# Performance work log

Hardware: AMD Instinct MI355X
Metric: run time of the kernel (lower is better)

## Reference

```python
import jax, jax.numpy as jnp
import numpy as np

B, T, C, H = 4, 4096, 1024, 64  # batch, seq_len, embedding_dimension, head_size


def setup_inputs() -> dict:
    key = jax.random.key(0)
    kx, kq, kk, kv = jax.random.split(key, 4)
    x = jax.random.normal(kx, (B, T, C), dtype=jnp.float32)
    # nn.Linear(C, H, bias=False) -> weight applied as x @ W with W:[C,H]
    s = 1.0 / np.sqrt(C)
    Wq = jax.random.normal(kq, (C, H), dtype=jnp.float32) * s
    Wk = jax.random.normal(kk, (C, H), dtype=jnp.float32) * s
    Wv = jax.random.normal(kv, (C, H), dtype=jnp.float32) * s
    return {"x": x, "Wq": Wq, "Wk": Wk, "Wv": Wv}


def reference(x, Wq, Wk, Wv):
    Bx, Tx, Cx = x.shape
    q = x @ Wq  # [B,T,H]
    k = x @ Wk  # [B,T,H]
    v = x @ Wv  # [B,T,H]
    # NOTE: original scales by C**-0.5 (embedding dim), not head_size**-0.5
    wei = jnp.einsum('bqh,bkh->bqk', q, k) * (Cx ** -0.5)  # [B,T,T]
    causal = jnp.tril(jnp.ones((Tx, Tx), dtype=bool))
    wei = jnp.where(causal, wei, -jnp.inf)
    wei = jax.nn.softmax(wei, axis=-1)
    out = jnp.einsum('bqk,bkh->bqh', wei, v)  # [B,T,H]
    return out
```

## Files before the change

kernel.cpp:

```cpp
#include <hip/hip_runtime.h>
#include <math.h>

#define BATCH 4
#define SEQ   4096
#define EMB   1024
#define HDIM  64
#define NSPLIT 4

typedef __attribute__((ext_vector_type(8))) short bf16x8;
typedef __attribute__((ext_vector_type(4))) float f32x4;
typedef __attribute__((ext_vector_type(4))) unsigned int u32x4;

#define MFMA16(a, b, c) __builtin_amdgcn_mfma_f32_16x16x32_bf16(a, b, c, 0, 0, 0)

__device__ __forceinline__ unsigned short f2bf(float f) {
  unsigned int u = __float_as_uint(f);
  u = (u + 0x7FFFu + ((u >> 16) & 1u)) >> 16;
  return (unsigned short)u;
}

__device__ __forceinline__ float fexp2(float x) {
  float r;
  asm("v_exp_f32 %0, %1" : "=v"(r) : "v"(x));
  return r;
}

__global__ __launch_bounds__(256) void wt_kernel(
    const float* __restrict__ Wq, const float* __restrict__ Wk,
    const float* __restrict__ Wv, unsigned short* __restrict__ wt) {
  __shared__ float tile[64][65];
  const int bid = blockIdx.x;
  const int m = bid >> 4, kt = bid & 15;
  const float* W = (m == 0) ? Wq : (m == 1) ? Wk : Wv;
  const int tid = threadIdx.x;
  {
    const int r = tid >> 2, c4 = tid & 3;
    const float* src = W + (size_t)(kt * 64 + r) * 64 + c4 * 16;
#pragma unroll
    for (int j = 0; j < 4; ++j) {
      float4 a = *(const float4*)(src + j * 4);
      tile[r][c4 * 16 + j * 4 + 0] = a.x;
      tile[r][c4 * 16 + j * 4 + 1] = a.y;
      tile[r][c4 * 16 + j * 4 + 2] = a.z;
      tile[r][c4 * 16 + j * 4 + 3] = a.w;
    }
  }
  __syncthreads();
  {
    const int col = tid >> 2, kq = tid & 3;
    unsigned short o[16];
#pragma unroll
    for (int j = 0; j < 16; ++j) o[j] = f2bf(tile[kq * 16 + j][col]);
    unsigned short* dst = wt + (size_t)(m * 64 + col) * 1024 + kt * 64 + kq * 16;
    *(bf16x8*)(dst)     = *(bf16x8*)&o[0];
    *(bf16x8*)(dst + 8) = *(bf16x8*)&o[8];
  }
}

__global__ __launch_bounds__(512) void qkv_mfma_kernel(
    const float* __restrict__ x, const unsigned short* __restrict__ wt,
    unsigned short* __restrict__ qb, unsigned short* __restrict__ kb,
    unsigned short* __restrict__ vt) {
  __shared__ __align__(16) unsigned short xs[64 * 64];
  __shared__ __align__(16) unsigned short ws[192 * 64];
  const int tid  = threadIdx.x;
  const int lane = tid & 63, wid = tid >> 6;
  const int g = lane >> 4, p = lane & 15;
  const int mt = wid >> 2, wq = wid & 3;
  const size_t row0 = (size_t)blockIdx.x * 64;

  const int sr = tid >> 3, sc = tid & 7;
  const float* xp = x + (row0 + sr) * EMB + sc * 8;

  f32x4 acc[2][3];
#pragma unroll
  for (int rt = 0; rt < 2; ++rt)
#pragma unroll
    for (int ct = 0; ct < 3; ++ct) acc[rt][ct] = (f32x4){0.f, 0.f, 0.f, 0.f};

  float4 rx[2];
  bf16x8 rw[3];
#pragma unroll
  for (int j = 0; j < 2; ++j) rx[j] = *(const float4*)(xp + j * 4);
#pragma unroll
  for (int it = 0; it < 3; ++it) {
    int i = tid + it * 512, col = i >> 3, cc = i & 7;
    rw[it] = *(const bf16x8*)(wt + (size_t)col * 1024 + cc * 8);
  }

  for (int kc = 0; kc < 16; ++kc) {
    __syncthreads();
#pragma unroll
    for (int j = 0; j < 2; ++j) {
      ushort4 h;
      h.x = f2bf(rx[j].x); h.y = f2bf(rx[j].y);
      h.z = f2bf(rx[j].z); h.w = f2bf(rx[j].w);
      *(ushort4*)((char*)xs + ((sr * 128 + sc * 16 + j * 8) ^ ((sr & 7) << 4))) = h;
    }
#pragma unroll
    for (int it = 0; it < 3; ++it) {
      int i = tid + it * 512, col = i >> 3, cc = i & 7;
      *(bf16x8*)((char*)ws + ((col * 128 + cc * 16) ^ ((col & 7) << 4))) = rw[it];
    }
    if (kc < 15) {
      const float* xpn = xp + (kc + 1) * 64;
#pragma unroll
      for (int j = 0; j < 2; ++j) rx[j] = *(const float4*)(xpn + j * 4);
#pragma unroll
      for (int it = 0; it < 3; ++it) {
        int i = tid + it * 512, col = i >> 3, cc = i & 7;
        rw[it] = *(const bf16x8*)(wt + (size_t)col * 1024 + (kc + 1) * 64 + cc * 8);
      }
    }
    __syncthreads();
#pragma unroll
    for (int ks = 0; ks < 2; ++ks) {
      bf16x8 af[2];
#pragma unroll
      for (int rt = 0; rt < 2; ++rt) {
        int row = mt * 32 + rt * 16 + p;
        af[rt] = *(const bf16x8*)((char*)xs +
                 ((row * 128 + ks * 64 + g * 16) ^ ((row & 7) << 4)));
      }
#pragma unroll
      for (int ct = 0; ct < 3; ++ct) {
        int col = wq * 48 + ct * 16 + p;
        bf16x8 bfr = *(const bf16x8*)((char*)ws +
                     ((col * 128 + ks * 64 + g * 16) ^ ((col & 7) << 4)));
#pragma unroll
        for (int rt = 0; rt < 2; ++rt)
          acc[rt][ct] = MFMA16(af[rt], bfr, acc[rt][ct]);
      }
    }
  }

  const int b     = (int)(row0 >> 12);
  const int tbase = (int)(row0 & 4095);
  unsigned short* vtb = vt + (((size_t)b * 64 + (tbase >> 6)) * 64) * 64;
#pragma unroll
  for (int rt = 0; rt < 2; ++rt)
#pragma unroll
    for (int ct = 0; ct < 3; ++ct) {
      const int c0  = wq * 48 + ct * 16;
      const int mtx = c0 >> 6;
      const int col = (c0 & 63) + p;
#pragma unroll
      for (int r = 0; r < 4; ++r) {
        const int row = mt * 32 + rt * 16 + 4 * g + r;
        const float vf = acc[rt][ct][r];
        if (mtx == 0)      qb[(row0 + row) * HDIM + col] = f2bf(vf * 0.0450843714f);
        else if (mtx == 1) kb[(row0 + row) * HDIM + col] = f2bf(vf);
        else               vtb[(size_t)col * 64 + row]   = f2bf(vf);
      }
    }
}

__device__ __forceinline__ void tile_body_lds(
    const unsigned short* __restrict__ sKb, const unsigned short* __restrict__ sVb,
    int qrel, bool diag,
    const bf16x8& qf0, const bf16x8& qf1,
    int p, int g, int cA0, int cA1, int srcA, int srcB, bool hi,
    float& m, float& l, f32x4 (&o)[4]) {
  f32x4 sc4[4];
#pragma unroll
  for (int t = 0; t < 4; ++t) {
    const int row = 16 * t + p;
    bf16x8 a0 = *(const bf16x8*)((const char*)sKb + row * 128 + cA0);
    bf16x8 a1 = *(const bf16x8*)((const char*)sKb + row * 128 + cA1);
    f32x4 a = (f32x4){0.f, 0.f, 0.f, 0.f};
    a = MFMA16(a0, qf0, a);
    a = MFMA16(a1, qf1, a);
    sc4[t] = a;
  }
  if (diag) {
#pragma unroll
    for (int t = 0; t < 4; ++t)
#pragma unroll
      for (int r = 0; r < 4; ++r)
        if (16 * t + 4 * g + r > qrel) sc4[t][r] = -1e30f;
  }
  float tm = -3e38f;
#pragma unroll
  for (int t = 0; t < 4; ++t)
#pragma unroll
    for (int r = 0; r < 4; ++r) tm = fmaxf(tm, sc4[t][r]);
  tm = fmaxf(tm, __shfl_xor(tm, 16));
  tm = fmaxf(tm, __shfl_xor(tm, 32));
  if (__any(tm > m + 11.5f)) {
    float mn = fmaxf(m, tm);
    float c = fexp2(m - mn);
    l *= c;
#pragma unroll
    for (int mi = 0; mi < 4; ++mi) o[mi] *= c;
    m = mn;
  }
  float psum = 0.f;
#pragma unroll
  for (int t = 0; t < 4; ++t)
#pragma unroll
    for (int r = 0; r < 4; ++r) {
      float pv = fexp2(sc4[t][r] - m);
      sc4[t][r] = pv;
      psum += pv;
    }
  l += psum;
  unsigned int pk[4][2];
#pragma unroll
  for (int t = 0; t < 4; ++t) {
    asm("v_cvt_pk_bf16_f32 %0, %1, %2"
        : "=v"(pk[t][0]) : "v"(sc4[t][0]), "v"(sc4[t][1]));
    asm("v_cvt_pk_bf16_f32 %0, %1, %2"
        : "=v"(pk[t][1]) : "v"(sc4[t][2]), "v"(sc4[t][3]));
  }
  u32x4 wb0, wb1;
#pragma unroll
  for (int h2 = 0; h2 < 2; ++h2) {
    const int src = h2 ? srcB : srcA;
    unsigned c0 = (unsigned)__shfl((int)pk[0][0], src);
    unsigned c1 = (unsigned)__shfl((int)pk[1][0], src);
    wb0[2 * h2 + 0] = hi ? c1 : c0;
    unsigned d0 = (unsigned)__shfl((int)pk[0][1], src);
    unsigned d1 = (unsigned)__shfl((int)pk[1][1], src);
    wb0[2 * h2 + 1] = hi ? d1 : d0;
    unsigned e0 = (unsigned)__shfl((int)pk[2][0], src);
    unsigned e1 = (unsigned)__shfl((int)pk[3][0], src);
    wb1[2 * h2 + 0] = hi ? e1 : e0;
    unsigned f0 = (unsigned)__shfl((int)pk[2][1], src);
    unsigned f1 = (unsigned)__shfl((int)pk[3][1], src);
    wb1[2 * h2 + 1] = hi ? f1 : f0;
  }
  bf16x8 b0 = __builtin_bit_cast(bf16x8, wb0);
  bf16x8 b1 = __builtin_bit_cast(bf16x8, wb1);
#pragma unroll
  for (int mi = 0; mi < 4; ++mi) {
    const int rowv = 16 * mi + p;
    bf16x8 va0 = *(const bf16x8*)((const char*)sVb + rowv * 128 + cA0);
    bf16x8 va1 = *(const bf16x8*)((const char*)sVb + rowv * 128 + cA1);
    o[mi] = MFMA16(va0, b0, o[mi]);
    o[mi] = MFMA16(va1, b1, o[mi]);
  }
}

__device__ __forceinline__ void item_map128(int g_it, int nA, int nB,
                                            int& kt, bool& isA, bool& diag) {
  if (g_it < nA) { isA = true;  kt = g_it;      diag = (kt >= nA - 2); }
  else           { isA = false; kt = g_it - nA; diag = (kt >= nB - 2); }
}

__global__ __launch_bounds__(512) void attn_partial_kernel(
    const unsigned short* __restrict__ qb, const unsigned short* __restrict__ kbm,
    const unsigned short* __restrict__ vt, float* __restrict__ pw) {
  __shared__ __align__(16) unsigned short sK[2][4096];
  __shared__ __align__(16) unsigned short sV[2][4096];
  const int tid = threadIdx.x;
  const int wid = tid >> 6, lane = tid & 63;
  const int g = lane >> 4, p = lane & 15;
  const int bid = blockIdx.x;
  const int sp = bid & 3, j = (bid >> 2) & 15, b = bid >> 6;
  const int jB = 31 - j;
  const int nA = 2 * j + 2, nB = 64 - 2 * j;
  const int tq0A = j * 128 + 16 * wid;
  const int tq0B = jB * 128 + 16 * wid;

  const char* kbase = (const char*)(kbm + (size_t)b * SEQ * HDIM);
  const char* vbase = (const char*)(vt  + (size_t)b * SEQ * HDIM);

  const unsigned short* qrowA = qb + ((size_t)b * SEQ + tq0A + p) * HDIM;
  const bf16x8 qfA0 = *(const bf16x8*)(qrowA + 8 * g);
  const bf16x8 qfA1 = *(const bf16x8*)(qrowA + 32 + 8 * g);
  const unsigned short* qrowB = qb + ((size_t)b * SEQ + tq0B + p) * HDIM;
  const bf16x8 qfB0 = *(const bf16x8*)(qrowB + 8 * g);
  const bf16x8 qfB1 = *(const bf16x8*)(qrowB + 32 + 8 * g);

  const int slot = tid * 16;
  const int r0 = slot >> 7, koff = r0 * 128 + ((slot & 127) ^ ((r0 & 7) << 4));

  const int swz = (p & 7) << 4;
  const int cA0 = (16 * g) ^ swz, cA1 = (64 + 16 * g) ^ swz;

  const int srcA = (g & 1) * 32 + p;
  const int srcB = srcA + 16;
  const bool hi = (g >> 1) != 0;

  float mA = -1e30f, lA = 0.f, mB = -1e30f, lB = 0.f;
  f32x4 oA[4], oB[4];
#pragma unroll
  for (int mi = 0; mi < 4; ++mi) {
    oA[mi] = (f32x4){0.f, 0.f, 0.f, 0.f};
    oB[mi] = (f32x4){0.f, 0.f, 0.f, 0.f};
  }

  const int cnt = (66 - sp + NSPLIT - 1) / NSPLIT;

  bf16x8 rk0, rv0;
  {
    int kt; bool isA, diag;
    item_map128(sp, nA, nB, kt, isA, diag);
    rk0 = *(const bf16x8*)(kbase + (size_t)kt * 8192 + koff);
    rv0 = *(const bf16x8*)(vbase + (size_t)kt * 8192 + koff);
  }
  *(bf16x8*)((char*)sK[0] + slot) = rk0;
  *(bf16x8*)((char*)sV[0] + slot) = rv0;
  if (cnt > 1) {
    int kt; bool isA, diag;
    item_map128(sp + NSPLIT, nA, nB, kt, isA, diag);
    rk0 = *(const bf16x8*)(kbase + (size_t)kt * 8192 + koff);
    rv0 = *(const bf16x8*)(vbase + (size_t)kt * 8192 + koff);
  }
  __syncthreads();

  for (int ii = 0; ii < cnt; ++ii) {
    const int buf = ii & 1;
    if (ii + 1 < cnt) {
      const int nb = buf ^ 1;
      *(bf16x8*)((char*)sK[nb] + slot) = rk0;
      *(bf16x8*)((char*)sV[nb] + slot) = rv0;
    }
    if (ii + 2 < cnt) {
      int kt; bool isA, diag;
      item_map128(sp + (ii + 2) * NSPLIT, nA, nB, kt, isA, diag);
      rk0 = *(const bf16x8*)(kbase + (size_t)kt * 8192 + koff);
      rv0 = *(const bf16x8*)(vbase + (size_t)kt * 8192 + koff);
    }
    int kt; bool isA, diag;
    item_map128(sp + ii * NSPLIT, nA, nB, kt, isA, diag);
    if (isA) {
      tile_body_lds(sK[buf], sV[buf], tq0A + p - kt * 64, diag, qfA0, qfA1,
                    p, g, cA0, cA1, srcA, srcB, hi, mA, lA, oA);
    } else {
      tile_body_lds(sK[buf], sV[buf], tq0B + p - kt * 64, diag, qfB0, qfB1,
                    p, g, cA0, cA1, srcA, srcB, hi, mB, lB, oB);
    }
    __syncthreads();
  }

  lA += __shfl_xor(lA, 16); lA += __shfl_xor(lA, 32);
  lB += __shfl_xor(lB, 16); lB += __shfl_xor(lB, 32);

  {
    const int grpA = j * 8 + wid;
    float* pp = pw + ((size_t)(b * 256 + grpA) * NSPLIT + sp) * 1056;
#pragma unroll
    for (int mi = 0; mi < 4; ++mi)
      *(f32x4*)(pp + p * 64 + 16 * mi + 4 * g) = oA[mi];
    if (g == 0) { pp[1024 + p] = mA; pp[1040 + p] = lA; }
  }
  {
    const int grpB = jB * 8 + wid;
    float* pp = pw + ((size_t)(b * 256 + grpB) * NSPLIT + sp) * 1056;
#pragma unroll
    for (int mi = 0; mi < 4; ++mi)
      *(f32x4*)(pp + p * 64 + 16 * mi + 4 * g) = oB[mi];
    if (g == 0) { pp[1024 + p] = mB; pp[1040 + p] = lB; }
  }
}

__global__ __launch_bounds__(256) void attn_merge_kernel(
    const float* __restrict__ pw, float* __restrict__ out) {
  const int bid = blockIdx.x;
  const int b = bid >> 8, grp = bid & 255;
  const int q = threadIdx.x & 15, db = threadIdx.x >> 4;
  const float* pp = pw + (size_t)bid * NSPLIT * 1056;
  float ms[NSPLIT], ls[NSPLIT];
  float mm = -3e38f;
#pragma unroll
  for (int s = 0; s < NSPLIT; ++s) {
    ms[s] = pp[s * 1056 + 1024 + q];
    ls[s] = pp[s * 1056 + 1040 + q];
    mm = fmaxf(mm, ms[s]);
  }
  float L = 0.f, a0 = 0.f, a1 = 0.f, a2 = 0.f, a3 = 0.f;
#pragma unroll
  for (int s = 0; s < NSPLIT; ++s) {
    float sc = fexp2(ms[s] - mm);
    L += ls[s] * sc;
    float4 v = *(const float4*)(pp + s * 1056 + q * 64 + 4 * db);
    a0 += v.x * sc; a1 += v.y * sc; a2 += v.z * sc; a3 += v.w * sc;
  }
  const float inv = 1.f / L;
  float* op = out + ((size_t)b * SEQ + grp * 16 + q) * HDIM + 4 * db;
  op[0] = a0 * inv; op[1] = a1 * inv; op[2] = a2 * inv; op[3] = a3 * inv;
}

extern "C" void kernel_launch(void* const* d_in, const int* in_sizes, int n_in,
                              void* d_out, int out_size, void* d_ws, size_t ws_size,
                              hipStream_t stream) {
  const float* x  = (const float*)d_in[0];
  const float* Wq = (const float*)d_in[1];
  const float* Wk = (const float*)d_in[2];
  const float* Wv = (const float*)d_in[3];
  float* outp = (float*)d_out;

  const size_t rows = (size_t)BATCH * SEQ;
  unsigned short* qbf = (unsigned short*)d_ws;
  unsigned short* kbf = qbf + rows * HDIM;
  unsigned short* vtb = kbf + rows * HDIM;
  unsigned short* wt  = vtb + rows * HDIM;
  float* pw = (float*)(wt + 192 * 1024);

  wt_kernel<<<dim3(48), dim3(256), 0, stream>>>(Wq, Wk, Wv, wt);
  qkv_mfma_kernel<<<dim3((unsigned)(rows / 64)), dim3(512), 0, stream>>>(x, wt, qbf, kbf, vtb);
  attn_partial_kernel<<<dim3(256), dim3(512), 0, stream>>>(qbf, kbf, vtb, pw);
  attn_merge_kernel<<<dim3(1024), dim3(256), 0, stream>>>(pw, outp);
}
```

Baseline: 58.00 us.

## Process K/V tiles in pairs with four LDS buffers to halve barriers

The attention partial kernel now keeps four LDS buffers for K and V instead of two and handles two key tiles per loop iteration. This halves the number of __syncthreads barriers and deepens register prefetch to two tiles ahead. In exchange, LDS use doubles to 64KB per block and more registers stay live, which may reduce occupancy.

```diff
diff --git a/kernel.cpp b/kernel.cpp
--- a/kernel.cpp
+++ b/kernel.cpp
@@ -250,8 +250,8 @@
 __global__ __launch_bounds__(512) void attn_partial_kernel(
     const unsigned short* __restrict__ qb, const unsigned short* __restrict__ kbm,
     const unsigned short* __restrict__ vt, float* __restrict__ pw) {
-  __shared__ __align__(16) unsigned short sK[2][4096];
-  __shared__ __align__(16) unsigned short sV[2][4096];
+  __shared__ __align__(16) unsigned short sK[4][4096];
+  __shared__ __align__(16) unsigned short sV[4][4096];
   const int tid = threadIdx.x;
   const int wid = tid >> 6, lane = tid & 63;
   const int g = lane >> 4, p = lane & 15;
@@ -292,47 +292,53 @@
 
   const int cnt = (66 - sp + NSPLIT - 1) / NSPLIT;
 
-  bf16x8 rk0, rv0;
-  {
-    int kt; bool isA, diag;
-    item_map128(sp, nA, nB, kt, isA, diag);
-    rk0 = *(const bf16x8*)(kbase + (size_t)kt * 8192 + koff);
-    rv0 = *(const bf16x8*)(vbase + (size_t)kt * 8192 + koff);
-  }
-  *(bf16x8*)((char*)sK[0] + slot) = rk0;
-  *(bf16x8*)((char*)sV[0] + slot) = rv0;
-  if (cnt > 1) {
-    int kt; bool isA, diag;
-    item_map128(sp + NSPLIT, nA, nB, kt, isA, diag);
-    rk0 = *(const bf16x8*)(kbase + (size_t)kt * 8192 + koff);
-    rv0 = *(const bf16x8*)(vbase + (size_t)kt * 8192 + koff);
-  }
+#define LOAD_ITEM(i, rk, rv) do {                                        \
+    int kt_; bool isA_, diag_;                                           \
+    item_map128(sp + (i) * NSPLIT, nA, nB, kt_, isA_, diag_);            \
+    rk = *(const bf16x8*)(kbase + (size_t)kt_ * 8192 + koff);            \
+    rv = *(const bf16x8*)(vbase + (size_t)kt_ * 8192 + koff);            \
+  } while (0)
+
+#define WRITE_BUF(bi, rk, rv) do {                                       \
+    *(bf16x8*)((char*)sK[bi] + slot) = rk;                               \
+    *(bf16x8*)((char*)sV[bi] + slot) = rv;                               \
+  } while (0)
+
+#define PROC_ITEM(i, bi) do {                                            \
+    int kt_; bool isA_, diag_;                                           \
+    item_map128(sp + (i) * NSPLIT, nA, nB, kt_, isA_, diag_);            \
+    if (isA_) tile_body_lds(sK[bi], sV[bi], tq0A + p - kt_ * 64, diag_,  \
+                            qfA0, qfA1, p, g, cA0, cA1, srcA, srcB, hi,  \
+                            mA, lA, oA);                                 \
+    else      tile_body_lds(sK[bi], sV[bi], tq0B + p - kt_ * 64, diag_,  \
+                            qfB0, qfB1, p, g, cA0, cA1, srcA, srcB, hi,  \
+                            mB, lB, oB);                                 \
+  } while (0)
+
+  bf16x8 rka, rva, rkb, rvb;
+  LOAD_ITEM(0, rka, rva);
+  WRITE_BUF(0, rka, rva);
+  if (cnt > 1) { LOAD_ITEM(1, rkb, rvb); WRITE_BUF(1, rkb, rvb); }
+  if (cnt > 2) LOAD_ITEM(2, rka, rva);
+  if (cnt > 3) LOAD_ITEM(3, rkb, rvb);
   __syncthreads();
 
-  for (int ii = 0; ii < cnt; ++ii) {
-    const int buf = ii & 1;
-    if (ii + 1 < cnt) {
-      const int nb = buf ^ 1;
-      *(bf16x8*)((char*)sK[nb] + slot) = rk0;
-      *(bf16x8*)((char*)sV[nb] + slot) = rv0;
-    }
-    if (ii + 2 < cnt) {
-      int kt; bool isA, diag;
-      item_map128(sp + (ii + 2) * NSPLIT, nA, nB, kt, isA, diag);
-      rk0 = *(const bf16x8*)(kbase + (size_t)kt * 8192 + koff);
-      rv0 = *(const bf16x8*)(vbase + (size_t)kt * 8192 + koff);
-    }
-    int kt; bool isA, diag;
-    item_map128(sp + ii * NSPLIT, nA, nB, kt, isA, diag);
-    if (isA) {
-      tile_body_lds(sK[buf], sV[buf], tq0A + p - kt * 64, diag, qfA0, qfA1,
-                    p, g, cA0, cA1, srcA, srcB, hi, mA, lA, oA);
-    } else {
-      tile_body_lds(sK[buf], sV[buf], tq0B + p - kt * 64, diag, qfB0, qfB1,
-                    p, g, cA0, cA1, srcA, srcB, hi, mB, lB, oB);
-    }
+  const int npairs = (cnt + 1) >> 1;
+  for (int pr = 0; pr < npairs; ++pr) {
+    const int base = (pr & 1) * 2, nxt = base ^ 2;
+    const int i0 = 2 * pr, i1 = 2 * pr + 1;
+    if (i0 + 2 < cnt) WRITE_BUF(nxt + 0, rka, rva);
+    if (i1 + 2 < cnt) WRITE_BUF(nxt + 1, rkb, rvb);
+    if (i0 + 4 < cnt) LOAD_ITEM(i0 + 4, rka, rva);
+    if (i1 + 4 < cnt) LOAD_ITEM(i1 + 4, rkb, rvb);
+    PROC_ITEM(i0, base + 0);
+    if (i1 < cnt) PROC_ITEM(i1, base + 1);
     __syncthreads();
   }
+
+#undef LOAD_ITEM
+#undef WRITE_BUF
+#undef PROC_ITEM
 
   lA += __shfl_xor(lA, 16); lA += __shfl_xor(lA, 32);
   lB += __shfl_xor(lB, 16); lB += __shfl_xor(lB, 32);
```

Measured after the change: 58.27 us. About the same (+0.5%).

## Switch attention to 32x32 MFMA tiles with waves split across query sides

Applied to the files above, without the earlier changes.

Replaces the 16x16x32 MFMA attention tile body with 32x32x16 MFMA, where each wave owns 32 queries. The eight waves are now split so four handle side A and four handle side B, instead of every wave processing both sides. This is meant to cut LDS fragment loads and cross-lane shuffles per FLOP and to halve per-wave accumulator state. The cost is that waves idle on tiles belonging to the other side, which may create load imbalance, since side A has fewer tiles than side B for most blocks.

```diff
diff --git a/kernel.cpp b/kernel.cpp
--- a/kernel.cpp
+++ b/kernel.cpp
@@ -9,9 +9,12 @@
 
 typedef __attribute__((ext_vector_type(8))) short bf16x8;
 typedef __attribute__((ext_vector_type(4))) float f32x4;
+typedef __attribute__((ext_vector_type(16))) float f32x16;
 typedef __attribute__((ext_vector_type(4))) unsigned int u32x4;
 
 #define MFMA16(a, b, c) __builtin_amdgcn_mfma_f32_16x16x32_bf16(a, b, c, 0, 0, 0)
+#define MFMA32(a, b, c) __builtin_amdgcn_mfma_f32_32x32x16_bf16(a, b, c, 0, 0, 0)
+#define ZERO16 (f32x16){0.f,0.f,0.f,0.f,0.f,0.f,0.f,0.f,0.f,0.f,0.f,0.f,0.f,0.f,0.f,0.f}
 
 __device__ __forceinline__ unsigned short f2bf(float f) {
   unsigned int u = __float_as_uint(f);
@@ -155,89 +158,76 @@
     }
 }
 
-__device__ __forceinline__ void tile_body_lds(
+__device__ __forceinline__ void tile_body32(
     const unsigned short* __restrict__ sKb, const unsigned short* __restrict__ sVb,
-    int qrel, bool diag,
-    const bf16x8& qf0, const bf16x8& qf1,
-    int p, int g, int cA0, int cA1, int srcA, int srcB, bool hi,
-    float& m, float& l, f32x4 (&o)[4]) {
-  f32x4 sc4[4];
-#pragma unroll
-  for (int t = 0; t < 4; ++t) {
-    const int row = 16 * t + p;
-    bf16x8 a0 = *(const bf16x8*)((const char*)sKb + row * 128 + cA0);
-    bf16x8 a1 = *(const bf16x8*)((const char*)sKb + row * 128 + cA1);
-    f32x4 a = (f32x4){0.f, 0.f, 0.f, 0.f};
-    a = MFMA16(a0, qf0, a);
-    a = MFMA16(a1, qf1, a);
-    sc4[t] = a;
+    int qrel, bool diag, const bf16x8 (&qf)[4], int h, int q5,
+    float& m, float& l, f32x16& o0, f32x16& o1) {
+  const int sw = (q5 & 7) << 4;
+  f32x16 s0 = ZERO16, s1 = ZERO16;
+#pragma unroll
+  for (int st = 0; st < 4; ++st) {
+    bf16x8 k0 = *(const bf16x8*)((const char*)sKb + q5 * 128 +
+                                 ((32 * st + 16 * h) ^ sw));
+    bf16x8 k1 = *(const bf16x8*)((const char*)sKb + (32 + q5) * 128 +
+                                 ((32 * st + 16 * h) ^ sw));
+    s0 = MFMA32(k0, qf[st], s0);
+    s1 = MFMA32(k1, qf[st], s1);
   }
   if (diag) {
 #pragma unroll
-    for (int t = 0; t < 4; ++t)
-#pragma unroll
-      for (int r = 0; r < 4; ++r)
-        if (16 * t + 4 * g + r > qrel) sc4[t][r] = -1e30f;
+    for (int r = 0; r < 16; ++r) {
+      const int kk = (r & 3) + 8 * (r >> 2) + 4 * h;
+      if (kk      > qrel) s0[r] = -1e30f;
+      if (kk + 32 > qrel) s1[r] = -1e30f;
+    }
   }
   float tm = -3e38f;
 #pragma unroll
-  for (int t = 0; t < 4; ++t)
-#pragma unroll
-    for (int r = 0; r < 4; ++r) tm = fmaxf(tm, sc4[t][r]);
-  tm = fmaxf(tm, __shfl_xor(tm, 16));
+  for (int r = 0; r < 16; ++r) { tm = fmaxf(tm, s0[r]); tm = fmaxf(tm, s1[r]); }
   tm = fmaxf(tm, __shfl_xor(tm, 32));
   if (__any(tm > m + 11.5f)) {
     float mn = fmaxf(m, tm);
     float c = fexp2(m - mn);
-    l *= c;
-#pragma unroll
-    for (int mi = 0; mi < 4; ++mi) o[mi] *= c;
+    l *= c; o0 *= c; o1 *= c;
     m = mn;
   }
-  float psum = 0.f;
-#pragma unroll
-  for (int t = 0; t < 4; ++t)
-#pragma unroll
-    for (int r = 0; r < 4; ++r) {
-      float pv = fexp2(sc4[t][r] - m);
-      sc4[t][r] = pv;
-      psum += pv;
-    }
-  l += psum;
-  unsigned int pk[4][2];
-#pragma unroll
-  for (int t = 0; t < 4; ++t) {
-    asm("v_cvt_pk_bf16_f32 %0, %1, %2"
-        : "=v"(pk[t][0]) : "v"(sc4[t][0]), "v"(sc4[t][1]));
-    asm("v_cvt_pk_bf16_f32 %0, %1, %2"
-        : "=v"(pk[t][1]) : "v"(sc4[t][2]), "v"(sc4[t][3]));
-  }
-  u32x4 wb0, wb1;
-#pragma unroll
-  for (int h2 = 0; h2 < 2; ++h2) {
-    const int src = h2 ? srcB : srcA;
-    unsigned c0 = (unsigned)__shfl((int)pk[0][0], src);
-    unsigned c1 = (unsigned)__shfl((int)pk[1][0], src);
-    wb0[2 * h2 + 0] = hi ? c1 : c0;
-    unsigned d0 = (unsigned)__shfl((int)pk[0][1], src);
-    unsigned d1 = (unsigned)__shfl((int)pk[1][1], src);
-    wb0[2 * h2 + 1] = hi ? d1 : d0;
-    unsigned e0 = (unsigned)__shfl((int)pk[2][0], src);
-    unsigned e1 = (unsigned)__shfl((int)pk[3][0], src);
-    wb1[2 * h2 + 0] = hi ? e1 : e0;
-    unsigned f0 = (unsigned)__shfl((int)pk[2][1], src);
-    unsigned f1 = (unsigned)__shfl((int)pk[3][1], src);
-    wb1[2 * h2 + 1] = hi ? f1 : f0;
-  }
-  bf16x8 b0 = __builtin_bit_cast(bf16x8, wb0);
-  bf16x8 b1 = __builtin_bit_cast(bf16x8, wb1);
-#pragma unroll
-  for (int mi = 0; mi < 4; ++mi) {
-    const int rowv = 16 * mi + p;
-    bf16x8 va0 = *(const bf16x8*)((const char*)sVb + rowv * 128 + cA0);
-    bf16x8 va1 = *(const bf16x8*)((const char*)sVb + rowv * 128 + cA1);
-    o[mi] = MFMA16(va0, b0, o[mi]);
-    o[mi] = MFMA16(va1, b1, o[mi]);
+  float ps = 0.f;
+#pragma unroll
+  for (int r = 0; r < 16; ++r) {
+    float a = fexp2(s0[r] - m); s0[r] = a; ps += a;
+    float c2 = fexp2(s1[r] - m); s1[r] = c2; ps += c2;
+  }
+  ps += __shfl_xor(ps, 32);
+  l += ps;
+  unsigned W[16];
+#pragma unroll
+  for (int i = 0; i < 8; ++i) {
+    asm("v_cvt_pk_bf16_f32 %0, %1, %2" : "=v"(W[i])     : "v"(s0[2*i]), "v"(s0[2*i+1]));
+    asm("v_cvt_pk_bf16_f32 %0, %1, %2" : "=v"(W[8 + i]) : "v"(s1[2*i]), "v"(s1[2*i+1]));
+  }
+  bf16x8 pf[4];
+#pragma unroll
+  for (int sG = 0; sG < 4; ++sG) {
+    const int ba = 4 * sG;
+    unsigned x0 = (unsigned)__shfl_xor((int)W[ba + 0], 32);
+    unsigned x1 = (unsigned)__shfl_xor((int)W[ba + 1], 32);
+    unsigned x2 = (unsigned)__shfl_xor((int)W[ba + 2], 32);
+    unsigned x3 = (unsigned)__shfl_xor((int)W[ba + 3], 32);
+    u32x4 fw;
+    fw[0] = h ? x2 : W[ba + 0];
+    fw[1] = h ? x3 : W[ba + 1];
+    fw[2] = h ? W[ba + 2] : x0;
+    fw[3] = h ? W[ba + 3] : x1;
+    pf[sG] = __builtin_bit_cast(bf16x8, fw);
+  }
+#pragma unroll
+  for (int sG = 0; sG < 4; ++sG) {
+    bf16x8 v0 = *(const bf16x8*)((const char*)sVb + q5 * 128 +
+                                 ((32 * sG + 16 * h) ^ sw));
+    o0 = MFMA32(v0, pf[sG], o0);
+    bf16x8 v1 = *(const bf16x8*)((const char*)sVb + (32 + q5) * 128 +
+                                 ((32 * sG + 16 * h) ^ sw));
+    o1 = MFMA32(v1, pf[sG], o1);
   }
 }
 
@@ -254,41 +244,31 @@
   __shared__ __align__(16) unsigned short sV[2][4096];
   const int tid = threadIdx.x;
   const int wid = tid >> 6, lane = tid & 63;
-  const int g = lane >> 4, p = lane & 15;
+  const int q5 = lane & 31, h = lane >> 5;
   const int bid = blockIdx.x;
   const int sp = bid & 3, j = (bid >> 2) & 15, b = bid >> 6;
   const int jB = 31 - j;
   const int nA = 2 * j + 2, nB = 64 - 2 * j;
-  const int tq0A = j * 128 + 16 * wid;
-  const int tq0B = jB * 128 + 16 * wid;
+  const bool sideA = (wid < 4);
+  const int ws = sideA ? wid : wid - 4;
+  const int tq0 = sideA ? j * 128 + 32 * ws : jB * 128 + 32 * ws;
 
   const char* kbase = (const char*)(kbm + (size_t)b * SEQ * HDIM);
   const char* vbase = (const char*)(vt  + (size_t)b * SEQ * HDIM);
 
-  const unsigned short* qrowA = qb + ((size_t)b * SEQ + tq0A + p) * HDIM;
-  const bf16x8 qfA0 = *(const bf16x8*)(qrowA + 8 * g);
-  const bf16x8 qfA1 = *(const bf16x8*)(qrowA + 32 + 8 * g);
-  const unsigned short* qrowB = qb + ((size_t)b * SEQ + tq0B + p) * HDIM;
-  const bf16x8 qfB0 = *(const bf16x8*)(qrowB + 8 * g);
-  const bf16x8 qfB1 = *(const bf16x8*)(qrowB + 32 + 8 * g);
+  bf16x8 qf[4];
+  {
+    const unsigned short* qrow = qb + ((size_t)b * SEQ + tq0 + q5) * HDIM;
+#pragma unroll
+    for (int st = 0; st < 4; ++st)
+      qf[st] = *(const bf16x8*)(qrow + 16 * st + 8 * h);
+  }
 
   const int slot = tid * 16;
   const int r0 = slot >> 7, koff = r0 * 128 + ((slot & 127) ^ ((r0 & 7) << 4));
 
-  const int swz = (p & 7) << 4;
-  const int cA0 = (16 * g) ^ swz, cA1 = (64 + 16 * g) ^ swz;
-
-  const int srcA = (g & 1) * 32 + p;
-  const int srcB = srcA + 16;
-  const bool hi = (g >> 1) != 0;
-
-  float mA = -1e30f, lA = 0.f, mB = -1e30f, lB = 0.f;
-  f32x4 oA[4], oB[4];
-#pragma unroll
-  for (int mi = 0; mi < 4; ++mi) {
-    oA[mi] = (f32x4){0.f, 0.f, 0.f, 0.f};
-    oB[mi] = (f32x4){0.f, 0.f, 0.f, 0.f};
-  }
+  float m = -1e30f, l = 0.f;
+  f32x16 o0 = ZERO16, o1 = ZERO16;
 
   const int cnt = (66 - sp + NSPLIT - 1) / NSPLIT;
 
@@ -324,35 +304,27 @@
     }
     int kt; bool isA, diag;
     item_map128(sp + ii * NSPLIT, nA, nB, kt, isA, diag);
-    if (isA) {
-      tile_body_lds(sK[buf], sV[buf], tq0A + p - kt * 64, diag, qfA0, qfA1,
-                    p, g, cA0, cA1, srcA, srcB, hi, mA, lA, oA);
-    } else {
-      tile_body_lds(sK[buf], sV[buf], tq0B + p - kt * 64, diag, qfB0, qfB1,
-                    p, g, cA0, cA1, srcA, srcB, hi, mB, lB, oB);
+    if (isA == sideA) {
+      tile_body32(sK[buf], sV[buf], tq0 + q5 - kt * 64, diag, qf, h, q5,
+                  m, l, o0, o1);
     }
     __syncthreads();
   }
 
-  lA += __shfl_xor(lA, 16); lA += __shfl_xor(lA, 32);
-  lB += __shfl_xor(lB, 16); lB += __shfl_xor(lB, 32);
-
-  {
-    const int grpA = j * 8 + wid;
-    float* pp = pw + ((size_t)(b * 256 + grpA) * NSPLIT + sp) * 1056;
-#pragma unroll
-    for (int mi = 0; mi < 4; ++mi)
-      *(f32x4*)(pp + p * 64 + 16 * mi + 4 * g) = oA[mi];
-    if (g == 0) { pp[1024 + p] = mA; pp[1040 + p] = lA; }
-  }
-  {
-    const int grpB = jB * 8 + wid;
-    float* pp = pw + ((size_t)(b * 256 + grpB) * NSPLIT + sp) * 1056;
-#pragma unroll
-    for (int mi = 0; mi < 4; ++mi)
-      *(f32x4*)(pp + p * 64 + 16 * mi + 4 * g) = oB[mi];
-    if (g == 0) { pp[1024 + p] = mB; pp[1040 + p] = lB; }
-  }
+  l += __shfl_xor(l, 32);
+  l *= 0.5f;
+
+  const int grp = (sideA ? j * 8 + 2 * ws : jB * 8 + 2 * ws) + (q5 >> 4);
+  float* pp = pw + ((size_t)(b * 256 + grp) * NSPLIT + sp) * 1056;
+  const int qr = (q5 & 15) * 64;
+#pragma unroll
+  for (int quad = 0; quad < 4; ++quad) {
+    *(f32x4*)(pp + qr + 8 * quad + 4 * h) =
+        (f32x4){o0[4 * quad], o0[4 * quad + 1], o0[4 * quad + 2], o0[4 * quad + 3]};
+    *(f32x4*)(pp + qr + 32 + 8 * quad + 4 * h) =
+        (f32x4){o1[4 * quad], o1[4 * quad + 1], o1[4 * quad + 2], o1[4 * quad + 3]};
+  }
+  if (h == 0) { pp[1024 + (q5 & 15)] = m; pp[1040 + (q5 & 15)] = l; }
 }
 
 __global__ __launch_bounds__(256) void attn_merge_kernel(
```

Result: faster. 56.61 us, median of 2 (-2.4%).
